# Kernel optimization log

Hardware: AMD Instinct MI355X
Metric: run time of the kernel (lower is better)

Reference implementation:

```python
import jax, jax.numpy as jnp
import numpy as np

V_PATCH_NUMS = (1, 2, 4, 6, 8, 10, 13, 16)
HW = 16
QUANT_RESI = 0.5
SHARE_K = 4
BETA = 1.0


def _pool_matrix(n_in, n_out):
    # adaptive average pooling as a [n_out, n_in] matrix (matches F.adaptive_avg_pool2d bins)
    P = np.zeros((n_out, n_in), np.float32)
    for i in range(n_out):
        s = (i * n_in) // n_out
        e = -((-(i + 1) * n_in) // n_out)  # ceil((i+1)*n_in/n_out)
        P[i, s:e] = 1.0 / (e - s)
    return jnp.asarray(P)


def _phi_index(si, SN):
    # PhiPartiallyShared.__getitem__(si/(SN-1)) with K=4 ticks
    K = SHARE_K
    ticks = np.linspace(1.0 / 3 / K, 1 - 1.0 / 3 / K, K) if K == 4 else np.linspace(1.0 / 2 / K, 1 - 1.0 / 2 / K, K)
    return int(np.argmin(np.abs(ticks - si / (SN - 1))))


def _phi(h, w, b):
    # Phi: h*(1-r) + conv3x3(h)*r, zero padding (nn.Conv2d default)
    y = jax.lax.conv_general_dilated(h, w, (1, 1), 'SAME',
                                     dimension_numbers=('NCHW', 'OIHW', 'NCHW'))
    y = y + b[None, :, None, None]
    return h * (1.0 - QUANT_RESI) + y * QUANT_RESI


def setup_inputs() -> dict:
    key = jax.random.key(0)
    k0, k1, k2 = jax.random.split(key, 3)
    B, C, V = 64, 32, 4096
    f = jax.random.normal(k0, (B, C, HW, HW), jnp.float32)
    embed = jax.random.normal(k1, (V, C), jnp.float32)  # EMAEmbedding.weight ~ randn
    phi_w = jax.random.normal(k2, (SHARE_K, C, C, 3, 3), jnp.float32) * (1.0 / np.sqrt(9.0 * C))
    phi_b = jnp.zeros((SHARE_K, C), jnp.float32)
    return {"f_BChw": f, "embed_weight": embed, "phi_w": phi_w, "phi_b": phi_b}


def reference(f_BChw, embed_weight, phi_w, phi_b):
    B, C, H, W = f_BChw.shape
    SN = len(V_PATCH_NUMS)
    f_ng = jax.lax.stop_gradient(f_BChw)
    f_hat = jnp.zeros_like(f_BChw)
    e_sq = jnp.sum(embed_weight * embed_weight, axis=1)  # [V]
    loss = jnp.float32(0.0)
    for si, pn in enumerate(V_PATCH_NUMS):
        rest = f_ng - jax.lax.stop_gradient(f_hat)  # residual to quantize (no grad through distance)
        if pn != H:
            P = _pool_matrix(H, pn)
            rest_d = jnp.einsum('oh,bchw,pw->bcop', P, rest, P)  # adaptive avg pool -> [B,C,pn,pn]
        else:
            rest_d = rest
        rest_NC = rest_d.transpose(0, 2, 3, 1).reshape(-1, C)  # [B*pn*pn, C]
        # squared euclidean cdist to codebook, argmin
        d = (jnp.sum(rest_NC * rest_NC, axis=1, keepdims=True)
             + e_sq[None, :]
             - 2.0 * (rest_NC @ embed_weight.T))  # [N, V]
        idx = jnp.argmin(d, axis=1)  # [B*pn*pn] int
        h = embed_weight[idx].reshape(B, pn, pn, C).transpose(0, 3, 1, 2)  # gather -> [B,C,pn,pn]
        if pn != H:
            h = jax.image.resize(h, (B, C, H, W), method='linear')  # bilinear, align_corners=False
        k = _phi_index(si, SN)
        h = _phi(h, phi_w[k], phi_b[k])
        f_hat = f_hat + h
        loss = loss + 0.25 * jnp.mean((jax.lax.stop_gradient(f_hat) - f_BChw) ** 2) \
                    + BETA * jnp.mean((f_hat - f_ng) ** 2)
    loss = loss / SN
    # straight-through estimator: grads flow to f_BChw as identity
    f_hat_st = jax.lax.stop_gradient(f_hat - f_BChw) + f_BChw
    return f_hat_st, loss
```

## Files before the change

kernel.cpp:

```cpp
#include <hip/hip_runtime.h>
#include <hip/hip_bf16.h>

#define BB 64
#define CC 32
#define HW2 256
#define VV 4096
#define NELEM (BB*CC*HW2)
#define PADW 18
#define PADA 324

#define OFF_F     0
#define OFF_FHAT  (OFF_F     + NELEM)
#define OFF_EMBT  (OFF_FHAT  + NELEM)
#define OFF_ESQ   (OFF_EMBT  + VV*CC)
#define OFF_PW    (OFF_ESQ   + VV)
#define OFF_PB    (OFF_PW    + 4*CC*CC*9)
#define OFF_REST  (OFF_PB    + 4*CC)
#define OFF_BESTA (OFF_REST  + 16384*CC)
#define OFF_BESTB (OFF_BESTA + 2*16384)
#define OFF_LOSS  (OFF_BESTB + 2*16384)
#define OFF_FLAG  (OFF_LOSS  + 1)

__device__ __forceinline__ int embt_idx(int v, int c) {
    return (v >> 6) * 2048 + c * 64 + (v & 63);
}

__global__ void k_probe(const void* __restrict__ fin, int* __restrict__ flag) {
    __shared__ int cnt[256];
    int t = threadIdx.x;
    const __hip_bfloat16* p = (const __hip_bfloat16*)fin;
    int local = 0;
    for (int i = t; i < 8192; i += 256) {
        float v = __bfloat162float(p[i]);
        if (!(fabsf(v) < 1e3f)) local++;
    }
    cnt[t] = local;
    __syncthreads();
    for (int s = 128; s > 0; s >>= 1) {
        if (t < s) cnt[t] += cnt[t + s];
        __syncthreads();
    }
    if (t == 0) *flag = (cnt[0] >= 64) ? 1 : 0;
}

__global__ void k_prep(const void* __restrict__ fin,
                       const void* __restrict__ ein,
                       const void* __restrict__ win,
                       const void* __restrict__ bin_,
                       const int* __restrict__ flag,
                       float* __restrict__ f, float* __restrict__ fhat,
                       float* __restrict__ embT, float* __restrict__ pw,
                       float* __restrict__ pb, float* __restrict__ loss) {
    bool isf32 = (*flag != 0);
    int i = blockIdx.x * 256 + threadIdx.x;
    if (i < NELEM) {
        f[i] = isf32 ? ((const float*)fin)[i]
                     : __bfloat162float(((const __hip_bfloat16*)fin)[i]);
        fhat[i] = 0.f;
    }
    if (i < VV*CC) {
        float ev = isf32 ? ((const float*)ein)[i]
                         : __bfloat162float(((const __hip_bfloat16*)ein)[i]);
        int v = i >> 5, c = i & 31;
        embT[embt_idx(v, c)] = ev;
    }
    if (i < 4*CC*CC*9)
        pw[i] = isf32 ? ((const float*)win)[i]
                      : __bfloat162float(((const __hip_bfloat16*)win)[i]);
    if (i < 4*CC)
        pb[i] = isf32 ? ((const float*)bin_)[i]
                      : __bfloat162float(((const __hip_bfloat16*)bin_)[i]);
    if (i == 0) *loss = 0.f;
}

__global__ void k_esq(const float* __restrict__ embT, float* __restrict__ esq) {
    int v = blockIdx.x * 256 + threadIdx.x;
    if (v >= VV) return;
    const float* p = embT + (v >> 6) * 2048 + (v & 63);
    float s = 0.f;
    #pragma unroll
    for (int c = 0; c < CC; ++c) { float e = p[c * 64]; s = fmaf(e, e, s); }
    esq[v] = s;
}

__global__ void k_pool0(const float* __restrict__ f, const float* __restrict__ fhat,
                        float* __restrict__ rest, unsigned long long* __restrict__ best) {
    int n = threadIdx.x;
    int c = blockIdx.y;
    if (n >= BB) return;
    if (c == 0) best[n] = 0xFFFFFFFFFFFFFFFFull;
    const float* fb = f + (n * CC + c) * HW2;
    const float* hb = fhat + (n * CC + c) * HW2;
    float s = 0.f;
    for (int h = 0; h < 16; ++h)
        for (int w = 0; w < 16; ++w)
            s += fb[h * 16 + w] - hb[h * 16 + w];
    rest[n * CC + c] = s * (1.f / 256.f);
}

__global__ __launch_bounds__(256)
void k_argmin(const float* __restrict__ rest, const float* __restrict__ embT,
              const float* __restrict__ esq, unsigned long long* __restrict__ best,
              int Ntot, int cpw) {
    __shared__ float xT[CC][132];
    __shared__ float eT[CC * 64];
    __shared__ float xxs[2][128];
    int tid = threadIdx.x;
    int tx = tid & 15, ty = tid >> 4;
    int qblk = blockIdx.x * 128;
    int v0 = blockIdx.y * cpw;
    int t0 = v0 >> 6;

    {
        int q = tid >> 1, h = tid & 1;
        int qq = qblk + q; if (qq > Ntot - 1) qq = Ntot - 1;
        const float* xr = rest + qq * CC + h * 16;
        float part = 0.f;
        #pragma unroll
        for (int c = 0; c < 16; ++c) {
            float xv = xr[c];
            xT[h * 16 + c][q] = xv;
            part = fmaf(xv, xv, part);
        }
        xxs[h][q] = part;
    }
    __syncthreads();

    float xx[8];
    #pragma unroll
    for (int i = 0; i < 8; ++i) {
        int q = ty * 8 + i;
        xx[i] = xxs[0][q] + xxs[1][q];
    }

    float bd[8]; int bi[8];
    #pragma unroll
    for (int i = 0; i < 8; ++i) { bd[i] = 3.4e38f; bi[i] = v0; }

    int ntiles = cpw >> 6;
    const float* gt0 = embT + (size_t)t0 * 2048;
    float4 s0 = *(const float4*)(gt0 + tid * 4);
    float4 s1 = *(const float4*)(gt0 + 1024 + tid * 4);

    for (int t = 0; t < ntiles; ++t) {
        int vbase = v0 + t * 64;
        __syncthreads();
        *(float4*)(eT + tid * 4) = s0;
        *(float4*)(eT + 1024 + tid * 4) = s1;
        __syncthreads();
        if (t + 1 < ntiles) {
            const float* gt = embT + (size_t)(t0 + t + 1) * 2048;
            s0 = *(const float4*)(gt + tid * 4);
            s1 = *(const float4*)(gt + 1024 + tid * 4);
        }

        float acc[8][4];
        #pragma unroll
        for (int i = 0; i < 8; ++i)
            #pragma unroll
            for (int j = 0; j < 4; ++j) acc[i][j] = 0.f;

        #pragma unroll 8
        for (int k = 0; k < CC; ++k) {
            float4 a0 = *(const float4*)&xT[k][ty * 8];
            float4 a1 = *(const float4*)&xT[k][ty * 8 + 4];
            float4 b4 = *(const float4*)&eT[k * 64 + tx * 4];
            float a[8] = {a0.x, a0.y, a0.z, a0.w, a1.x, a1.y, a1.z, a1.w};
            float b[4] = {b4.x, b4.y, b4.z, b4.w};
            #pragma unroll
            for (int i = 0; i < 8; ++i)
                #pragma unroll
                for (int j = 0; j < 4; ++j)
                    acc[i][j] = fmaf(a[i], b[j], acc[i][j]);
        }

        float4 es4 = *(const float4*)(esq + vbase + tx * 4);
        float es[4] = {es4.x, es4.y, es4.z, es4.w};
        #pragma unroll
        for (int i = 0; i < 8; ++i) {
            float base = xx[i];
            #pragma unroll
            for (int j = 0; j < 4; ++j) {
                float dist = fmaf(-2.f, acc[i][j], base + es[j]);
                if (dist < bd[i]) { bd[i] = dist; bi[i] = vbase + tx * 4 + j; }
            }
        }
    }

    #pragma unroll
    for (int i = 0; i < 8; ++i) {
        unsigned u = __float_as_uint(bd[i]);
        unsigned long long mono = (u & 0x80000000u)
            ? (unsigned long long)(~u)
            : (unsigned long long)(u | 0x80000000u);
        unsigned long long pk = (mono << 32) | (unsigned long long)(unsigned)bi[i];
        #pragma unroll
        for (int m = 1; m <= 8; m <<= 1) {
            unsigned long long o = __shfl_xor(pk, m, 64);
            if (o < pk) pk = o;
        }
        int q = qblk + ty * 8 + i;
        if (tx == 0 && q < Ntot)
            atomicMin(best + q, pk);
    }
}

__global__ __launch_bounds__(256)
void k_fuse(const float* __restrict__ embT,
            const unsigned long long* __restrict__ best,
            const float* __restrict__ pw, const float* __restrict__ pb,
            const float* __restrict__ f, float* __restrict__ fhat,
            float* __restrict__ loss,
            float* __restrict__ rest,
            unsigned long long* __restrict__ best_next,
            int pn, int k, int pn_next) {
    __shared__ float h_pad[CC * PADA];
    __shared__ float extra[CC * 169];
    __shared__ float red[4];
    int b = blockIdx.x, co8 = blockIdx.y, t = threadIdx.x;
    int nn = pn * pn;
    int y = t >> 4, x = t & 15;

    for (int i = t; i < CC * 68; i += 256) {
        int c = i / 68, r = i % 68;
        int pos;
        if (r < 18)      pos = r;
        else if (r < 36) pos = 17 * PADW + (r - 18);
        else if (r < 52) pos = (r - 35) * PADW;
        else             pos = (r - 51) * PADW + 17;
        h_pad[c * PADA + pos] = 0.f;
    }

    if (pn == 16) {
        int id = (int)(unsigned)(best[b * HW2 + t] & 0xFFFFFFFFull);
        const float* er = embT + (id >> 6) * 2048 + (id & 63);
        int ctr = (y + 1) * PADW + (x + 1);
        #pragma unroll
        for (int c = 0; c < CC; ++c)
            h_pad[c * PADA + ctr] = er[c * 64];
    } else {
        float (*hs)[169] = (float(*)[169])extra;
        for (int cell = t; cell < nn; cell += 256) {
            int id = (int)(unsigned)(best[b * nn + cell] & 0xFFFFFFFFull);
            const float* er = embT + (id >> 6) * 2048 + (id & 63);
            #pragma unroll
            for (int c = 0; c < CC; ++c) hs[c][cell] = er[c * 64];
        }
        __syncthreads();
        float scale = (float)pn / 16.f;
        float sy = (y + 0.5f) * scale - 0.5f;
        sy = fminf(fmaxf(sy, 0.f), (float)(pn - 1));
        int y0 = (int)sy; int y1 = min(y0 + 1, pn - 1); float wy = sy - (float)y0;
        float sx = (x + 0.5f) * scale - 0.5f;
        sx = fminf(fmaxf(sx, 0.f), (float)(pn - 1));
        int x0 = (int)sx; int x1 = min(x0 + 1, pn - 1); float wx = sx - (float)x0;
        float wy0 = 1.f - wy, wx0 = 1.f - wx;
        int ctr = (y + 1) * PADW + (x + 1);
        #pragma unroll
        for (int c = 0; c < CC; ++c) {
            float v00 = hs[c][y0 * pn + x0], v01 = hs[c][y0 * pn + x1];
            float v10 = hs[c][y1 * pn + x0], v11 = hs[c][y1 * pn + x1];
            float a0 = wy0 * v00 + wy * v10;
            float a1 = wy0 * v01 + wy * v11;
            h_pad[c * PADA + ctr] = wx0 * a0 + wx * a1;
        }
    }
    __syncthreads();

    int posb = (b * CC + co8 * 4) * HW2 + t;
    float fh_pre[4], f_pre[4];
    #pragma unroll
    for (int o = 0; o < 4; ++o) {
        fh_pre[o] = fhat[posb + o * HW2];
        f_pre[o]  = f[posb + o * HW2];
    }

    float acc[4];
    #pragma unroll
    for (int o = 0; o < 4; ++o) acc[o] = 0.f;
    const float* hbase = h_pad + y * PADW + x;
    const float* wpk = pw + (k * CC + co8 * 4) * (CC * 9);
    #pragma unroll
    for (int ci_ = 0; ci_ < CC; ++ci_) {
        float hv[9];
        #pragma unroll
        for (int dy = 0; dy < 3; ++dy)
            #pragma unroll
            for (int dx = 0; dx < 3; ++dx)
                hv[dy * 3 + dx] = hbase[ci_ * PADA + dy * PADW + dx];
        const float* wp = wpk + ci_ * 9;
        #pragma unroll
        for (int o = 0; o < 4; ++o) {
            const float* w9 = wp + o * (CC * 9);
            #pragma unroll
            for (int q = 0; q < 9; ++q) acc[o] = fmaf(hv[q], w9[q], acc[o]);
        }
    }

    float* diff = extra;
    float lsum = 0.f;
    int ctr = (y + 1) * PADW + (x + 1);
    #pragma unroll
    for (int o = 0; o < 4; ++o) {
        int co = co8 * 4 + o;
        float hval = h_pad[co * PADA + ctr];
        float outv = hval * 0.5f + (acc[o] + pb[k * CC + co]) * 0.5f;
        float fh = fh_pre[o] + outv;
        fhat[posb + o * HW2] = fh;
        float dd = f_pre[o] - fh;
        diff[o * HW2 + t] = dd;
        lsum = fmaf(dd, dd, lsum);
    }
    #pragma unroll
    for (int off = 32; off > 0; off >>= 1) lsum += __shfl_down(lsum, off, 64);
    if ((t & 63) == 0) red[t >> 6] = lsum;
    __syncthreads();
    if (t == 0)
        atomicAdd(loss, red[0] + red[1] + red[2] + red[3]);

    if (pn_next > 0) {
        int nn2 = pn_next * pn_next;
        for (int q = t; q < nn2 * 4; q += 256) {
            int cell = q % nn2, o = q / nn2;
            int i = cell / pn_next, j = cell % pn_next;
            int s0 = (i * 16) / pn_next, e0 = ((i + 1) * 16 + pn_next - 1) / pn_next;
            int s1 = (j * 16) / pn_next, e1 = ((j + 1) * 16 + pn_next - 1) / pn_next;
            float inv = 1.f / (float)((e0 - s0) * (e1 - s1));
            float s = 0.f;
            for (int h = s0; h < e0; ++h)
                for (int w = s1; w < e1; ++w)
                    s += diff[o * HW2 + h * 16 + w];
            rest[(b * nn2 + cell) * CC + co8 * 4 + o] = s * inv;
        }
        if (co8 == 0)
            for (int q = t; q < nn2; q += 256)
                best_next[b * nn2 + q] = 0xFFFFFFFFFFFFFFFFull;
    }
}

__global__ void k_out(const float* __restrict__ fhat, const float* __restrict__ loss,
                      const int* __restrict__ flag, void* __restrict__ out) {
    bool isf32 = (*flag != 0);
    int i = blockIdx.x * 256 + threadIdx.x;
    if (i > NELEM) return;
    float v;
    if (i < NELEM) v = fhat[i];
    else           v = (*loss) * (1.25f / (float)NELEM / 8.f);
    if (isf32) ((float*)out)[i] = v;
    else       ((__hip_bfloat16*)out)[i] = __float2bfloat16(v);
}

extern "C" void kernel_launch(void* const* d_in, const int* in_sizes, int n_in,
                              void* d_out, int out_size, void* d_ws, size_t ws_size,
                              hipStream_t stream) {
    const void* fin  = d_in[0];
    const void* ein  = d_in[1];
    const void* win  = d_in[2];
    const void* bin_ = d_in[3];
    float* ws = (float*)d_ws;
    float* f    = ws + OFF_F;
    float* fhat = ws + OFF_FHAT;
    float* embT = ws + OFF_EMBT;
    float* esq  = ws + OFF_ESQ;
    float* pw   = ws + OFF_PW;
    float* pb   = ws + OFF_PB;
    float* rest = ws + OFF_REST;
    unsigned long long* bestA = (unsigned long long*)(ws + OFF_BESTA);
    unsigned long long* bestB = (unsigned long long*)(ws + OFF_BESTB);
    float* loss = ws + OFF_LOSS;
    int*   flag = (int*)(ws + OFF_FLAG);

    static const int PN[8] = {1, 2, 4, 6, 8, 10, 13, 16};
    static const int KK[8] = {0, 0, 1, 1, 2, 2, 3, 3};
    static const int SP[8] = {64, 64, 64, 64, 32, 32, 16, 16};

    k_probe<<<1, 256, 0, stream>>>(fin, flag);
    k_prep<<<(NELEM + 255) / 256, 256, 0, stream>>>(fin, ein, win, bin_, flag,
                                                    f, fhat, embT, pw, pb, loss);
    k_esq<<<(VV + 255) / 256, 256, 0, stream>>>(embT, esq);
    k_pool0<<<dim3(1, CC), 256, 0, stream>>>(f, fhat, rest, bestA);

    for (int si = 0; si < 8; ++si) {
        int pn = PN[si];
        int Ntot = BB * pn * pn;
        int Sp = SP[si];
        int cpw = VV / Sp;
        unsigned long long* bcur = (si & 1) ? bestB : bestA;
        unsigned long long* bnxt = (si & 1) ? bestA : bestB;
        int pn_next = (si < 7) ? PN[si + 1] : 0;
        int gx = (Ntot + 127) / 128;
        k_argmin<<<dim3(gx, Sp), 256, 0, stream>>>(rest, embT, esq, bcur, Ntot, cpw);
        k_fuse<<<dim3(BB, 8), 256, 0, stream>>>(embT, bcur, pw, pb, f, fhat, loss,
                                                rest, bnxt, pn, KK[si], pn_next);
    }
    k_out<<<(NELEM + 1 + 255) / 256, 256, 0, stream>>>(fhat, loss, flag, d_out);
}
```

Before: 459.8 us.

## Shrink k_fuse shared memory and split output channels across more blocks

The fuse kernel now runs 16 blocks per batch item with 2 output channels each, instead of 8 blocks with 4. The separate 'extra' shared buffer is removed: the low-res codebook tile is staged in h_pad, the interpolated values are held in registers, and the padded tile is rebuilt after a barrier. This cuts shared memory per block and adds parallelism, aiming for higher occupancy. The cost is that each block redoes the gather, interpolation and halo fill for half as many channels, so that redundant work doubles.

```diff
diff --git a/kernel.cpp b/kernel.cpp
--- a/kernel.cpp
+++ b/kernel.cpp
@@ -215,31 +215,30 @@
             unsigned long long* __restrict__ best_next,
             int pn, int k, int pn_next) {
     __shared__ float h_pad[CC * PADA];
-    __shared__ float extra[CC * 169];
+    __shared__ float diff[2 * HW2];
     __shared__ float red[4];
-    int b = blockIdx.x, co8 = blockIdx.y, t = threadIdx.x;
+    int b = blockIdx.x, co16 = blockIdx.y, t = threadIdx.x;
     int nn = pn * pn;
     int y = t >> 4, x = t & 15;
-
-    for (int i = t; i < CC * 68; i += 256) {
-        int c = i / 68, r = i % 68;
-        int pos;
-        if (r < 18)      pos = r;
-        else if (r < 36) pos = 17 * PADW + (r - 18);
-        else if (r < 52) pos = (r - 35) * PADW;
-        else             pos = (r - 51) * PADW + 17;
-        h_pad[c * PADA + pos] = 0.f;
-    }
+    int ctr = (y + 1) * PADW + (x + 1);
 
     if (pn == 16) {
+        for (int i = t; i < CC * 68; i += 256) {
+            int c = i / 68, r = i % 68;
+            int pos;
+            if (r < 18)      pos = r;
+            else if (r < 36) pos = 17 * PADW + (r - 18);
+            else if (r < 52) pos = (r - 35) * PADW;
+            else             pos = (r - 51) * PADW + 17;
+            h_pad[c * PADA + pos] = 0.f;
+        }
         int id = (int)(unsigned)(best[b * HW2 + t] & 0xFFFFFFFFull);
         const float* er = embT + (id >> 6) * 2048 + (id & 63);
-        int ctr = (y + 1) * PADW + (x + 1);
         #pragma unroll
         for (int c = 0; c < CC; ++c)
             h_pad[c * PADA + ctr] = er[c * 64];
     } else {
-        float (*hs)[169] = (float(*)[169])extra;
+        float (*hs)[169] = (float(*)[169])h_pad;
         for (int cell = t; cell < nn; cell += 256) {
             int id = (int)(unsigned)(best[b * nn + cell] & 0xFFFFFFFFull);
             const float* er = embT + (id >> 6) * 2048 + (id & 63);
@@ -255,31 +254,42 @@
         sx = fminf(fmaxf(sx, 0.f), (float)(pn - 1));
         int x0 = (int)sx; int x1 = min(x0 + 1, pn - 1); float wx = sx - (float)x0;
         float wy0 = 1.f - wy, wx0 = 1.f - wx;
-        int ctr = (y + 1) * PADW + (x + 1);
+        float hval[CC];
         #pragma unroll
         for (int c = 0; c < CC; ++c) {
             float v00 = hs[c][y0 * pn + x0], v01 = hs[c][y0 * pn + x1];
             float v10 = hs[c][y1 * pn + x0], v11 = hs[c][y1 * pn + x1];
             float a0 = wy0 * v00 + wy * v10;
             float a1 = wy0 * v01 + wy * v11;
-            h_pad[c * PADA + ctr] = wx0 * a0 + wx * a1;
-        }
+            hval[c] = wx0 * a0 + wx * a1;
+        }
+        __syncthreads();
+        for (int i = t; i < CC * 68; i += 256) {
+            int c = i / 68, r = i % 68;
+            int pos;
+            if (r < 18)      pos = r;
+            else if (r < 36) pos = 17 * PADW + (r - 18);
+            else if (r < 52) pos = (r - 35) * PADW;
+            else             pos = (r - 51) * PADW + 17;
+            h_pad[c * PADA + pos] = 0.f;
+        }
+        #pragma unroll
+        for (int c = 0; c < CC; ++c)
+            h_pad[c * PADA + ctr] = hval[c];
     }
     __syncthreads();
 
-    int posb = (b * CC + co8 * 4) * HW2 + t;
-    float fh_pre[4], f_pre[4];
-    #pragma unroll
-    for (int o = 0; o < 4; ++o) {
+    int posb = (b * CC + co16 * 2) * HW2 + t;
+    float fh_pre[2], f_pre[2];
+    #pragma unroll
+    for (int o = 0; o < 2; ++o) {
         fh_pre[o] = fhat[posb + o * HW2];
         f_pre[o]  = f[posb + o * HW2];
     }
 
-    float acc[4];
-    #pragma unroll
-    for (int o = 0; o < 4; ++o) acc[o] = 0.f;
+    float acc[2] = {0.f, 0.f};
     const float* hbase = h_pad + y * PADW + x;
-    const float* wpk = pw + (k * CC + co8 * 4) * (CC * 9);
+    const float* wpk = pw + (k * CC + co16 * 2) * (CC * 9);
     #pragma unroll
     for (int ci_ = 0; ci_ < CC; ++ci_) {
         float hv[9];
@@ -288,21 +298,19 @@
             #pragma unroll
             for (int dx = 0; dx < 3; ++dx)
                 hv[dy * 3 + dx] = hbase[ci_ * PADA + dy * PADW + dx];
-        const float* wp = wpk + ci_ * 9;
-        #pragma unroll
-        for (int o = 0; o < 4; ++o) {
-            const float* w9 = wp + o * (CC * 9);
-            #pragma unroll
-            for (int q = 0; q < 9; ++q) acc[o] = fmaf(hv[q], w9[q], acc[o]);
-        }
-    }
-
-    float* diff = extra;
+        const float* w0 = wpk + ci_ * 9;
+        const float* w1 = w0 + CC * 9;
+        #pragma unroll
+        for (int q = 0; q < 9; ++q) {
+            acc[0] = fmaf(hv[q], w0[q], acc[0]);
+            acc[1] = fmaf(hv[q], w1[q], acc[1]);
+        }
+    }
+
     float lsum = 0.f;
-    int ctr = (y + 1) * PADW + (x + 1);
-    #pragma unroll
-    for (int o = 0; o < 4; ++o) {
-        int co = co8 * 4 + o;
+    #pragma unroll
+    for (int o = 0; o < 2; ++o) {
+        int co = co16 * 2 + o;
         float hval = h_pad[co * PADA + ctr];
         float outv = hval * 0.5f + (acc[o] + pb[k * CC + co]) * 0.5f;
         float fh = fh_pre[o] + outv;
@@ -320,7 +328,7 @@
 
     if (pn_next > 0) {
         int nn2 = pn_next * pn_next;
-        for (int q = t; q < nn2 * 4; q += 256) {
+        for (int q = t; q < nn2 * 2; q += 256) {
             int cell = q % nn2, o = q / nn2;
             int i = cell / pn_next, j = cell % pn_next;
             int s0 = (i * 16) / pn_next, e0 = ((i + 1) * 16 + pn_next - 1) / pn_next;
@@ -330,9 +338,9 @@
             for (int h = s0; h < e0; ++h)
                 for (int w = s1; w < e1; ++w)
                     s += diff[o * HW2 + h * 16 + w];
-            rest[(b * nn2 + cell) * CC + co8 * 4 + o] = s * inv;
-        }
-        if (co8 == 0)
+            rest[(b * nn2 + cell) * CC + co16 * 2 + o] = s * inv;
+        }
+        if (co16 == 0)
             for (int q = t; q < nn2; q += 256)
                 best_next[b * nn2 + q] = 0xFFFFFFFFFFFFFFFFull;
     }
@@ -390,8 +398,8 @@
         int pn_next = (si < 7) ? PN[si + 1] : 0;
         int gx = (Ntot + 127) / 128;
         k_argmin<<<dim3(gx, Sp), 256, 0, stream>>>(rest, embT, esq, bcur, Ntot, cpw);
-        k_fuse<<<dim3(BB, 8), 256, 0, stream>>>(embT, bcur, pw, pb, f, fhat, loss,
-                                                rest, bnxt, pn, KK[si], pn_next);
+        k_fuse<<<dim3(BB, 16), 256, 0, stream>>>(embT, bcur, pw, pb, f, fhat, loss,
+                                                 rest, bnxt, pn, KK[si], pn_next);
     }
     k_out<<<(NELEM + 1 + 255) / 256, 256, 0, stream>>>(fhat, loss, flag, d_out);
 }
```

Result: slower. 549.7 us (+19.5%).

## Track residual instead of f and f_hat, split upsample into separate kernel

Applied to the files above, without the earlier changes.

Replaces the separate f and f_hat buffers with a single residual buffer D = f - f_hat, which halves the per-stage reads and writes in the conv kernel and reconstructs f_hat at output as f - D. The fused gather/upsample+conv kernel is split. A new k_up kernel computes the upsampled codebook map once per batch into a channel-last buffer. This avoids each of the eight conv blocks redoing the gather and bilinear interpolation for all 32 channels. It adds an extra kernel launch and a global round-trip of the upsampled map per stage.

```diff
diff --git a/kernel.cpp b/kernel.cpp
--- a/kernel.cpp
+++ b/kernel.cpp
@@ -9,9 +9,8 @@
 #define PADW 18
 #define PADA 324
 
-#define OFF_F     0
-#define OFF_FHAT  (OFF_F     + NELEM)
-#define OFF_EMBT  (OFF_FHAT  + NELEM)
+#define OFF_D     0
+#define OFF_EMBT  (OFF_D     + NELEM)
 #define OFF_ESQ   (OFF_EMBT  + VV*CC)
 #define OFF_PW    (OFF_ESQ   + VV)
 #define OFF_PB    (OFF_PW    + 4*CC*CC*9)
@@ -20,9 +19,15 @@
 #define OFF_BESTB (OFF_BESTA + 2*16384)
 #define OFF_LOSS  (OFF_BESTB + 2*16384)
 #define OFF_FLAG  (OFF_LOSS  + 1)
+#define OFF_HUP   (OFF_FLAG  + 3)
 
 __device__ __forceinline__ int embt_idx(int v, int c) {
     return (v >> 6) * 2048 + c * 64 + (v & 63);
+}
+
+__device__ __forceinline__ float decf(const void* fin, bool isf32, int i) {
+    return isf32 ? ((const float*)fin)[i]
+                 : __bfloat162float(((const __hip_bfloat16*)fin)[i]);
 }
 
 __global__ void k_probe(const void* __restrict__ fin, int* __restrict__ flag) {
@@ -48,16 +53,14 @@
                        const void* __restrict__ win,
                        const void* __restrict__ bin_,
                        const int* __restrict__ flag,
-                       float* __restrict__ f, float* __restrict__ fhat,
+                       float* __restrict__ D,
                        float* __restrict__ embT, float* __restrict__ pw,
                        float* __restrict__ pb, float* __restrict__ loss) {
     bool isf32 = (*flag != 0);
     int i = blockIdx.x * 256 + threadIdx.x;
-    if (i < NELEM) {
-        f[i] = isf32 ? ((const float*)fin)[i]
+    if (i < NELEM)
+        D[i] = isf32 ? ((const float*)fin)[i]
                      : __bfloat162float(((const __hip_bfloat16*)fin)[i]);
-        fhat[i] = 0.f;
-    }
     if (i < VV*CC) {
         float ev = isf32 ? ((const float*)ein)[i]
                          : __bfloat162float(((const __hip_bfloat16*)ein)[i]);
@@ -83,18 +86,17 @@
     esq[v] = s;
 }
 
-__global__ void k_pool0(const float* __restrict__ f, const float* __restrict__ fhat,
+__global__ void k_pool0(const float* __restrict__ D,
                         float* __restrict__ rest, unsigned long long* __restrict__ best) {
     int n = threadIdx.x;
     int c = blockIdx.y;
     if (n >= BB) return;
     if (c == 0) best[n] = 0xFFFFFFFFFFFFFFFFull;
-    const float* fb = f + (n * CC + c) * HW2;
-    const float* hb = fhat + (n * CC + c) * HW2;
+    const float* fb = D + (n * CC + c) * HW2;
     float s = 0.f;
     for (int h = 0; h < 16; ++h)
         for (int w = 0; w < 16; ++w)
-            s += fb[h * 16 + w] - hb[h * 16 + w];
+            s += fb[h * 16 + w];
     rest[n * CC + c] = s * (1.f / 256.f);
 }
 
@@ -206,45 +208,27 @@
 }
 
 __global__ __launch_bounds__(256)
-void k_fuse(const float* __restrict__ embT,
-            const unsigned long long* __restrict__ best,
-            const float* __restrict__ pw, const float* __restrict__ pb,
-            const float* __restrict__ f, float* __restrict__ fhat,
-            float* __restrict__ loss,
-            float* __restrict__ rest,
-            unsigned long long* __restrict__ best_next,
-            int pn, int k, int pn_next) {
-    __shared__ float h_pad[CC * PADA];
-    __shared__ float extra[CC * 169];
-    __shared__ float red[4];
-    int b = blockIdx.x, co8 = blockIdx.y, t = threadIdx.x;
+void k_up(const float* __restrict__ embT,
+          const unsigned long long* __restrict__ best,
+          float* __restrict__ hup, int pn) {
+    __shared__ float hs[8][169];
+    int b = blockIdx.x, cg = blockIdx.y, t = threadIdx.x;
     int nn = pn * pn;
     int y = t >> 4, x = t & 15;
-
-    for (int i = t; i < CC * 68; i += 256) {
-        int c = i / 68, r = i % 68;
-        int pos;
-        if (r < 18)      pos = r;
-        else if (r < 36) pos = 17 * PADW + (r - 18);
-        else if (r < 52) pos = (r - 35) * PADW;
-        else             pos = (r - 51) * PADW + 17;
-        h_pad[c * PADA + pos] = 0.f;
-    }
+    int c0 = cg * 8;
+    float hv[8];
 
     if (pn == 16) {
         int id = (int)(unsigned)(best[b * HW2 + t] & 0xFFFFFFFFull);
         const float* er = embT + (id >> 6) * 2048 + (id & 63);
-        int ctr = (y + 1) * PADW + (x + 1);
-        #pragma unroll
-        for (int c = 0; c < CC; ++c)
-            h_pad[c * PADA + ctr] = er[c * 64];
+        #pragma unroll
+        for (int c = 0; c < 8; ++c) hv[c] = er[(c0 + c) * 64];
     } else {
-        float (*hs)[169] = (float(*)[169])extra;
         for (int cell = t; cell < nn; cell += 256) {
             int id = (int)(unsigned)(best[b * nn + cell] & 0xFFFFFFFFull);
             const float* er = embT + (id >> 6) * 2048 + (id & 63);
             #pragma unroll
-            for (int c = 0; c < CC; ++c) hs[c][cell] = er[c * 64];
+            for (int c = 0; c < 8; ++c) hs[c][cell] = er[(c0 + c) * 64];
         }
         __syncthreads();
         float scale = (float)pn / 16.f;
@@ -255,25 +239,61 @@
         sx = fminf(fmaxf(sx, 0.f), (float)(pn - 1));
         int x0 = (int)sx; int x1 = min(x0 + 1, pn - 1); float wx = sx - (float)x0;
         float wy0 = 1.f - wy, wx0 = 1.f - wx;
-        int ctr = (y + 1) * PADW + (x + 1);
-        #pragma unroll
-        for (int c = 0; c < CC; ++c) {
+        #pragma unroll
+        for (int c = 0; c < 8; ++c) {
             float v00 = hs[c][y0 * pn + x0], v01 = hs[c][y0 * pn + x1];
             float v10 = hs[c][y1 * pn + x0], v11 = hs[c][y1 * pn + x1];
             float a0 = wy0 * v00 + wy * v10;
             float a1 = wy0 * v01 + wy * v11;
-            h_pad[c * PADA + ctr] = wx0 * a0 + wx * a1;
+            hv[c] = wx0 * a0 + wx * a1;
+        }
+    }
+    float* hp = hup + (b * HW2 + t) * CC + c0;
+    *(float4*)hp       = make_float4(hv[0], hv[1], hv[2], hv[3]);
+    *(float4*)(hp + 4) = make_float4(hv[4], hv[5], hv[6], hv[7]);
+}
+
+__global__ __launch_bounds__(256)
+void k_conv(const float* __restrict__ hup,
+            const float* __restrict__ pw, const float* __restrict__ pb,
+            float* __restrict__ D,
+            float* __restrict__ loss,
+            float* __restrict__ rest,
+            unsigned long long* __restrict__ best_next,
+            int k, int pn_next) {
+    __shared__ float h_pad[CC * PADA];
+    __shared__ float diff[4 * HW2];
+    __shared__ float red[4];
+    int b = blockIdx.x, co8 = blockIdx.y, t = threadIdx.x;
+    int y = t >> 4, x = t & 15;
+    int ctr = (y + 1) * PADW + (x + 1);
+
+    for (int i = t; i < CC * 68; i += 256) {
+        int c = i / 68, r = i % 68;
+        int pos;
+        if (r < 18)      pos = r;
+        else if (r < 36) pos = 17 * PADW + (r - 18);
+        else if (r < 52) pos = (r - 35) * PADW;
+        else             pos = (r - 51) * PADW + 17;
+        h_pad[c * PADA + pos] = 0.f;
+    }
+    {
+        const float* hp = hup + (b * HW2 + t) * CC;
+        #pragma unroll
+        for (int s8 = 0; s8 < 8; ++s8) {
+            float4 e4 = *(const float4*)(hp + s8 * 4);
+            h_pad[(s8 * 4 + 0) * PADA + ctr] = e4.x;
+            h_pad[(s8 * 4 + 1) * PADA + ctr] = e4.y;
+            h_pad[(s8 * 4 + 2) * PADA + ctr] = e4.z;
+            h_pad[(s8 * 4 + 3) * PADA + ctr] = e4.w;
         }
     }
     __syncthreads();
 
     int posb = (b * CC + co8 * 4) * HW2 + t;
-    float fh_pre[4], f_pre[4];
-    #pragma unroll
-    for (int o = 0; o < 4; ++o) {
-        fh_pre[o] = fhat[posb + o * HW2];
-        f_pre[o]  = f[posb + o * HW2];
-    }
+    float D_pre[4];
+    #pragma unroll
+    for (int o = 0; o < 4; ++o) D_pre[o] = D[posb + o * HW2];
 
     float acc[4];
     #pragma unroll
@@ -297,17 +317,14 @@
         }
     }
 
-    float* diff = extra;
     float lsum = 0.f;
-    int ctr = (y + 1) * PADW + (x + 1);
     #pragma unroll
     for (int o = 0; o < 4; ++o) {
         int co = co8 * 4 + o;
         float hval = h_pad[co * PADA + ctr];
         float outv = hval * 0.5f + (acc[o] + pb[k * CC + co]) * 0.5f;
-        float fh = fh_pre[o] + outv;
-        fhat[posb + o * HW2] = fh;
-        float dd = f_pre[o] - fh;
+        float dd = D_pre[o] - outv;
+        D[posb + o * HW2] = dd;
         diff[o * HW2 + t] = dd;
         lsum = fmaf(dd, dd, lsum);
     }
@@ -338,13 +355,14 @@
     }
 }
 
-__global__ void k_out(const float* __restrict__ fhat, const float* __restrict__ loss,
-                      const int* __restrict__ flag, void* __restrict__ out) {
+__global__ void k_out(const float* __restrict__ D, const float* __restrict__ loss,
+                      const void* __restrict__ fin, const int* __restrict__ flag,
+                      void* __restrict__ out) {
     bool isf32 = (*flag != 0);
     int i = blockIdx.x * 256 + threadIdx.x;
     if (i > NELEM) return;
     float v;
-    if (i < NELEM) v = fhat[i];
+    if (i < NELEM) v = decf(fin, isf32, i) - D[i];
     else           v = (*loss) * (1.25f / (float)NELEM / 8.f);
     if (isf32) ((float*)out)[i] = v;
     else       ((__hip_bfloat16*)out)[i] = __float2bfloat16(v);
@@ -358,8 +376,7 @@
     const void* win  = d_in[2];
     const void* bin_ = d_in[3];
     float* ws = (float*)d_ws;
-    float* f    = ws + OFF_F;
-    float* fhat = ws + OFF_FHAT;
+    float* D    = ws + OFF_D;
     float* embT = ws + OFF_EMBT;
     float* esq  = ws + OFF_ESQ;
     float* pw   = ws + OFF_PW;
@@ -369,6 +386,7 @@
     unsigned long long* bestB = (unsigned long long*)(ws + OFF_BESTB);
     float* loss = ws + OFF_LOSS;
     int*   flag = (int*)(ws + OFF_FLAG);
+    float* hup  = ws + OFF_HUP;
 
     static const int PN[8] = {1, 2, 4, 6, 8, 10, 13, 16};
     static const int KK[8] = {0, 0, 1, 1, 2, 2, 3, 3};
@@ -376,9 +394,9 @@
 
     k_probe<<<1, 256, 0, stream>>>(fin, flag);
     k_prep<<<(NELEM + 255) / 256, 256, 0, stream>>>(fin, ein, win, bin_, flag,
-                                                    f, fhat, embT, pw, pb, loss);
+                                                    D, embT, pw, pb, loss);
     k_esq<<<(VV + 255) / 256, 256, 0, stream>>>(embT, esq);
-    k_pool0<<<dim3(1, CC), 256, 0, stream>>>(f, fhat, rest, bestA);
+    k_pool0<<<dim3(1, CC), 256, 0, stream>>>(D, rest, bestA);
 
     for (int si = 0; si < 8; ++si) {
         int pn = PN[si];
@@ -390,8 +408,9 @@
         int pn_next = (si < 7) ? PN[si + 1] : 0;
         int gx = (Ntot + 127) / 128;
         k_argmin<<<dim3(gx, Sp), 256, 0, stream>>>(rest, embT, esq, bcur, Ntot, cpw);
-        k_fuse<<<dim3(BB, 8), 256, 0, stream>>>(embT, bcur, pw, pb, f, fhat, loss,
-                                                rest, bnxt, pn, KK[si], pn_next);
-    }
-    k_out<<<(NELEM + 1 + 255) / 256, 256, 0, stream>>>(fhat, loss, flag, d_out);
-}
+        k_up<<<dim3(BB, 4), 256, 0, stream>>>(embT, bcur, hup, pn);
+        k_conv<<<dim3(BB, 8), 256, 0, stream>>>(hup, pw, pb, D, loss,
+                                                rest, bnxt, KK[si], pn_next);
+    }
+    k_out<<<(NELEM + 1 + 255) / 256, 256, 0, stream>>>(D, loss, fin, flag, d_out);
+}
```

New measurement: 462.9 us. No clear change (+0.7%).
